# Performance work log

Hardware: AMD Instinct MI355X
Metric: run time of the kernel (lower is better)

The kernel has to match this reference:

```python
import jax, jax.numpy as jnp
import numpy as np

B, S, E, H = 2, 2048, 1024, 16
D = E // H  # head_dim = 64
SCALE = 1.0 / np.sqrt(D)


def setup_inputs() -> dict:
    key = jax.random.key(0)
    ks = jax.random.split(key, 5)
    std = 0.02
    return {
        "x": jax.random.normal(ks[0], (B, S, E), dtype=jnp.float32),
        "wq": jax.random.normal(ks[1], (E, E), dtype=jnp.float32) * std,
        "wk": jax.random.normal(ks[2], (E, E), dtype=jnp.float32) * std,
        "wv": jax.random.normal(ks[3], (E, E), dtype=jnp.float32) * std,
        "wo": jax.random.normal(ks[4], (E, E), dtype=jnp.float32) * std,
    }


def reference(x, wq, wk, wv, wo):
    # Linear projections (torch Linear: y = x @ W.T); weights stored as [out, in]
    q = jnp.einsum('bse,fe->bsf', x, wq)
    k = jnp.einsum('bse,fe->bsf', x, wk)
    v = jnp.einsum('bse,fe->bsf', x, wv)
    # split heads -> [B, H, S, D]
    q = q.reshape(B, S, H, D).transpose(0, 2, 1, 3)
    k = k.reshape(B, S, H, D).transpose(0, 2, 1, 3)
    v = v.reshape(B, S, H, D).transpose(0, 2, 1, 3)
    # scaled dot-product scores [B, H, S, S]
    scores = jnp.einsum('bhqd,bhkd->bhqk', q, k) * SCALE
    # causal mask: -inf above diagonal
    causal = jnp.triu(jnp.full((S, S), -jnp.inf, dtype=scores.dtype), k=1)
    scores = scores + causal[None, None, :, :]
    attn = jax.nn.softmax(scores, axis=-1)
    # dropout p=0 -> identity
    out = jnp.einsum('bhqk,bhkd->bhqd', attn, v)
    out = out.transpose(0, 2, 1, 3).reshape(B, S, E)
    return jnp.einsum('bse,fe->bsf', out, wo)
```

## Files before the change

kernel.cpp:

```cpp
#include <hip/hip_runtime.h>
#include <hip/hip_bf16.h>

#define B_ 2
#define S_ 2048
#define E_ 1024
#define H_ 16
#define D_ 64
#define QKV_N 3072
#define C2_ 0.18033688011112042f

typedef __attribute__((ext_vector_type(8))) unsigned short ushort8_t;
typedef __attribute__((ext_vector_type(8))) short short8_t;
typedef __attribute__((ext_vector_type(4))) float f32x4;

__device__ __forceinline__ unsigned short f2b(float f) {
    union { float f; unsigned u; } x; x.f = f;
    unsigned r = x.u + 0x7FFFu + ((x.u >> 16) & 1u);
    return (unsigned short)(r >> 16);
}
__device__ __forceinline__ ushort2 pkbf(float a, float b) {
    union { __hip_bfloat162 h; ushort2 u; } c;
    c.h = __float22bfloat162_rn(make_float2(a, b));
    return c.u;
}
__device__ __forceinline__ void glds16(const unsigned short* g, unsigned short* l) {
    __builtin_amdgcn_global_load_lds((const __attribute__((address_space(1))) void*)g,
                                     (__attribute__((address_space(3))) void*)l, 16, 0, 0);
}

__global__ __launch_bounds__(256) void cast_all(const float* __restrict__ x,
                                                const float* __restrict__ wq,
                                                const float* __restrict__ wk,
                                                const float* __restrict__ wv,
                                                const float* __restrict__ wo,
                                                unsigned short* __restrict__ xb,
                                                unsigned short* __restrict__ wb) {
    int idx = blockIdx.x * 256 + threadIdx.x;
    const float* src; unsigned short* dst; float s = 1.f; int j;
    if (idx < 1048576) {
        src = x; dst = xb; j = idx;
    } else {
        j = idx - 1048576;
        int y = j >> 18;
        src = (y == 0) ? wq : (y == 1) ? wk : (y == 2) ? wv : wo;
        dst = wb + (size_t)y * 1048576;
        j &= 262143;
        if (y == 0) s = C2_;
    }
    float4 v = ((const float4*)src)[j];
    ushort2 lo = pkbf(v.x * s, v.y * s), hi = pkbf(v.z * s, v.w * s);
    ((ushort4*)dst)[j] = make_ushort4(lo.x, lo.y, hi.x, hi.y);
}

template <int TM, bool OUT_BF16, bool VT>
__device__ __forceinline__ void gemm_bt_body(const unsigned short* __restrict__ A,
                                             const unsigned short* __restrict__ Bt,
                                             void* __restrict__ Cout,
                                             int m0, int n0, int N, int K) {
    __shared__ unsigned short As[2 * TM * 32];
    __shared__ unsigned short Bs[2 * 128 * 32];
    const int tid = threadIdx.x;
    const int wave = tid >> 6;
    const int lane = tid & 63;
    const int wm = (wave >> 1) * (TM / 2);
    const int wn = (wave & 1) * 64;
    const int quad = lane >> 4;
    const int l15 = lane & 15;
    constexpr int MI = TM / 32;

    f32x4 acc[MI][4] = {};

    const int srow = lane >> 2;
    const int scb  = (lane & 3) * 8;
    const unsigned short* gB0 = Bt + (size_t)(n0 + wave * 32 + srow) * K + scb;
    const unsigned short* gB1 = gB0 + (size_t)16 * K;
    unsigned short* lB0 = Bs + wave * 1024;
    unsigned short* lB1 = lB0 + 512;
    const unsigned short* gA0;
    const unsigned short* gA1 = nullptr;
    unsigned short* lA0;
    unsigned short* lA1 = nullptr;
    if (TM == 128) {
        gA0 = A + (size_t)(m0 + wave * 32 + srow) * K + scb;
        gA1 = gA0 + (size_t)16 * K;
        lA0 = As + wave * 1024; lA1 = lA0 + 512;
    } else {
        gA0 = A + (size_t)(m0 + wave * 16 + srow) * K + scb;
        lA0 = As + wave * 512;
    }

    for (int k0 = 0; k0 < K; k0 += 64) {
        __syncthreads();
        glds16(gA0 + k0, lA0);
        glds16(gA0 + k0 + 32, lA0 + TM * 32);
        if (TM == 128) {
            glds16(gA1 + k0, lA1);
            glds16(gA1 + k0 + 32, lA1 + TM * 32);
        }
        glds16(gB0 + k0, lB0);
        glds16(gB0 + k0 + 32, lB0 + 128 * 32);
        glds16(gB1 + k0, lB1);
        glds16(gB1 + k0 + 32, lB1 + 128 * 32);
        __syncthreads();

#pragma unroll
        for (int h = 0; h < 2; ++h) {
            const unsigned short* ah = As + h * TM * 32;
            const unsigned short* bh = Bs + h * 128 * 32;
            short8_t af[MI], bfv[4];
#pragma unroll
            for (int mi = 0; mi < MI; ++mi)
                af[mi] = *(const short8_t*)(&ah[(wm + mi * 16 + l15) * 32 + quad * 8]);
#pragma unroll
            for (int ni = 0; ni < 4; ++ni)
                bfv[ni] = *(const short8_t*)(&bh[(wn + ni * 16 + l15) * 32 + quad * 8]);
#pragma unroll
            for (int mi = 0; mi < MI; ++mi)
#pragma unroll
                for (int ni = 0; ni < 4; ++ni)
                    acc[mi][ni] = __builtin_amdgcn_mfma_f32_16x16x32_bf16(
                        af[mi], bfv[ni], acc[mi][ni], 0, 0, 0);
        }
    }

    if (VT && n0 >= 2048) {
#pragma unroll
        for (int mi = 0; mi < MI; ++mi)
#pragma unroll
            for (int ni = 0; ni < 4; ++ni) {
                int col = n0 + wn + ni * 16 + l15;
                int r0  = m0 + wm + mi * 16 + quad * 4;
                int bb  = r0 >> 11, s = r0 & 2047;
                size_t drow = (size_t)bb * 2048 + 2 * (col - 2048) + (s >> 10);
                unsigned short* dp = (unsigned short*)Cout + drow * QKV_N + 2048 + (s & 1023);
                *(ushort4*)dp = make_ushort4(f2b(acc[mi][ni][0]), f2b(acc[mi][ni][1]),
                                             f2b(acc[mi][ni][2]), f2b(acc[mi][ni][3]));
            }
        return;
    }

#pragma unroll
    for (int mi = 0; mi < MI; ++mi)
#pragma unroll
        for (int ni = 0; ni < 4; ++ni)
#pragma unroll
            for (int r = 0; r < 4; ++r) {
                int row = m0 + wm + mi * 16 + quad * 4 + r;
                int col = n0 + wn + ni * 16 + l15;
                float val = acc[mi][ni][r];
                if (OUT_BF16)
                    ((unsigned short*)Cout)[(size_t)row * N + col] = f2b(val);
                else
                    ((float*)Cout)[(size_t)row * N + col] = val;
            }
}

__global__ __launch_bounds__(256, 3) void gemm_qkv(const unsigned short* __restrict__ xb,
                                                   const unsigned short* __restrict__ wqkv,
                                                   unsigned short* __restrict__ qkv) {
    int id = blockIdx.x + 24 * blockIdx.y;
    int sw = (id & 7) * 96 + (id >> 3);
    int n0 = (sw % 24) * 128;
    int m0 = (sw / 24) * 128;
    gemm_bt_body<128, true, true>(xb, wqkv, qkv, m0, n0, QKV_N, E_);
}

__global__ __launch_bounds__(256, 2) void gemm_out(const unsigned short* __restrict__ a,
                                                   const unsigned short* __restrict__ wob,
                                                   float* __restrict__ c) {
    gemm_bt_body<64, false, false>(a, wob, c, blockIdx.y * 64, blockIdx.x * 128, E_, E_);
}

__global__ __launch_bounds__(512, 4) void attn_kernel(const unsigned short* __restrict__ QKV,
                                                      unsigned short* __restrict__ O) {
    __shared__ unsigned short Ks[2][64 * 64];
    __shared__ unsigned short Vs[2][64 * 64];
    __shared__ unsigned short Ps[8][16 * 64];

    const int b = blockIdx.z, h = blockIdx.y;
    const int cx = blockIdx.x;
    const int c0 = (cx & 1) ? (15 - (cx >> 1)) : (cx >> 1);
    const int c = (b == 0) ? c0 : (15 - c0);
    const int tid = threadIdx.x;
    const int w = tid >> 6, lane = tid & 63;
    const int quad = lane >> 4, l15 = lane & 15;
    const int lx = l15 & 7;
    const int chunk = (w < 4) ? (31 - c) : c;
    const int Q0 = chunk * 64 + (w & 3) * 16;

    const size_t qo = (size_t)(b * S_ + Q0 + l15) * QKV_N + h * D_;
    short8_t bq0 = *(const short8_t*)(QKV + qo + quad * 8);
    short8_t bq1 = *(const short8_t*)(QKV + qo + 32 + quad * 8);

    f32x4 Oacc[4] = {};
    float lsum = 0.f;
    const int qg = Q0 + l15;

    const int fo0 = ((quad) ^ lx) * 8;
    const int fo1 = ((4 + quad) ^ lx) * 8;
    const int krow = l15 * 64;
    int pwo[4];
#pragma unroll
    for (int tm = 0; tm < 4; ++tm)
        pwo[tm] = ((tm * 2 + (quad >> 1)) ^ lx) * 8 + (quad & 1) * 4;

    const int srow = tid >> 3;
    const int scb  = tid & 7;
    const int swz  = (scb ^ (srow & 7)) * 8;
    const unsigned short* Kbase = QKV + (size_t)(b * S_) * QKV_N + 1024 + h * D_;
    const unsigned short* Vb2 = QKV + (size_t)(b * S_ + 2 * (h * D_ + srow)) * QKV_N + 2048;

    const int ntiles = 32 - c;
    const int nT = (ntiles + 1) >> 1;
    for (int t = 0; t < nT; ++t) {
        const int kt0 = t * 128;
        ushort8_t ka = *(const ushort8_t*)(Kbase + (size_t)(kt0 + srow) * QKV_N + scb * 8);
        ushort8_t kb = *(const ushort8_t*)(Kbase + (size_t)(kt0 + 64 + srow) * QKV_N + scb * 8);
        ushort8_t va = *(const ushort8_t*)(Vb2 + (size_t)(kt0 >> 10) * QKV_N
                                               + (kt0 & 1023) + scb * 8);
        ushort8_t vb = *(const ushort8_t*)(Vb2 + (size_t)((kt0 + 64) >> 10) * QKV_N
                                               + ((kt0 + 64) & 1023) + scb * 8);
        __syncthreads();
        *(ushort8_t*)(&Ks[0][srow * 64 + swz]) = ka;
        *(ushort8_t*)(&Ks[1][srow * 64 + swz]) = kb;
        *(ushort8_t*)(&Vs[0][srow * 64 + swz]) = va;
        *(ushort8_t*)(&Vs[1][srow * 64 + swz]) = vb;
        __syncthreads();

#pragma unroll
        for (int s = 0; s < 2; ++s) {
            const int kt = kt0 + s * 64;
            if (kt > Q0 + 15) continue;
            const bool h2 = (kt + 32 <= Q0 + 15);

            if (kt + 63 <= Q0) {
#pragma unroll
                for (int tm = 0; tm < 4; ++tm) {
                    short8_t ak0 = *(const short8_t*)(&Ks[s][tm * 1024 + krow + fo0]);
                    short8_t ak1 = *(const short8_t*)(&Ks[s][tm * 1024 + krow + fo1]);
                    f32x4 st = {0.f, 0.f, 0.f, 0.f};
                    st = __builtin_amdgcn_mfma_f32_16x16x32_bf16(ak0, bq0, st, 0, 0, 0);
                    st = __builtin_amdgcn_mfma_f32_16x16x32_bf16(ak1, bq1, st, 0, 0, 0);
                    float p0 = __builtin_amdgcn_exp2f(st[0]);
                    float p1 = __builtin_amdgcn_exp2f(st[1]);
                    float p2 = __builtin_amdgcn_exp2f(st[2]);
                    float p3 = __builtin_amdgcn_exp2f(st[3]);
                    lsum += (p0 + p1) + (p2 + p3);
                    ushort2 a = pkbf(p0, p1), c2 = pkbf(p2, p3);
                    *(ushort4*)(&Ps[w][krow + pwo[tm]]) = make_ushort4(a.x, a.y, c2.x, c2.y);
                }
            } else {
                const int need = h2 ? 4 : 2;
                for (int tm = 0; tm < need; ++tm) {
                    if (kt + tm * 16 <= Q0 + 15) {
                        short8_t ak0 = *(const short8_t*)(&Ks[s][tm * 1024 + krow + fo0]);
                        short8_t ak1 = *(const short8_t*)(&Ks[s][tm * 1024 + krow + fo1]);
                        f32x4 st = {0.f, 0.f, 0.f, 0.f};
                        st = __builtin_amdgcn_mfma_f32_16x16x32_bf16(ak0, bq0, st, 0, 0, 0);
                        st = __builtin_amdgcn_mfma_f32_16x16x32_bf16(ak1, bq1, st, 0, 0, 0);
                        const int kvb = kt + tm * 16 + quad * 4;
                        float p0 = (kvb     > qg) ? 0.f : __builtin_amdgcn_exp2f(st[0]);
                        float p1 = (kvb + 1 > qg) ? 0.f : __builtin_amdgcn_exp2f(st[1]);
                        float p2 = (kvb + 2 > qg) ? 0.f : __builtin_amdgcn_exp2f(st[2]);
                        float p3 = (kvb + 3 > qg) ? 0.f : __builtin_amdgcn_exp2f(st[3]);
                        lsum += (p0 + p1) + (p2 + p3);
                        ushort2 a = pkbf(p0, p1), c2 = pkbf(p2, p3);
                        *(ushort4*)(&Ps[w][krow + pwo[tm]]) = make_ushort4(a.x, a.y, c2.x, c2.y);
                    } else {
                        *(ushort4*)(&Ps[w][krow + pwo[tm]]) = make_ushort4(0, 0, 0, 0);
                    }
                }
            }

#pragma unroll
            for (int kh = 0; kh < 2; ++kh) {
                if (kh == 1 && !h2) break;
                const int fo = kh ? fo1 : fo0;
                short8_t bv[4];
#pragma unroll
                for (int tn = 0; tn < 4; ++tn)
                    bv[tn] = *(const short8_t*)(&Vs[s][tn * 1024 + krow + fo]);
                short8_t ap = *(const short8_t*)(&Ps[w][krow + fo]);
#pragma unroll
                for (int tn = 0; tn < 4; ++tn)
                    Oacc[tn] = __builtin_amdgcn_mfma_f32_16x16x32_bf16(
                        ap, bv[tn], Oacc[tn], 0, 0, 0);
            }
        }
    }

    float l = lsum;
    l += __shfl_xor(l, 16);
    l += __shfl_xor(l, 32);
    float inv = 1.f / l;
    float lir[4];
#pragma unroll
    for (int r = 0; r < 4; ++r)
        lir[r] = __shfl(inv, quad * 4 + r);
#pragma unroll
    for (int tn = 0; tn < 4; ++tn)
#pragma unroll
        for (int r = 0; r < 4; ++r) {
            int row = Q0 + quad * 4 + r;
            O[(size_t)(b * S_ + row) * E_ + h * D_ + tn * 16 + l15] =
                f2b(Oacc[tn][r] * lir[r]);
        }
}

extern "C" void kernel_launch(void* const* d_in, const int* in_sizes, int n_in,
                              void* d_out, int out_size, void* d_ws, size_t ws_size,
                              hipStream_t stream) {
    const float* x  = (const float*)d_in[0];
    const float* wq = (const float*)d_in[1];
    const float* wk = (const float*)d_in[2];
    const float* wv = (const float*)d_in[3];
    const float* wo = (const float*)d_in[4];
    float* out = (float*)d_out;

    unsigned short* ws   = (unsigned short*)d_ws;
    unsigned short* xb   = ws;
    unsigned short* wqkv = ws + 4194304;
    unsigned short* wob  = ws + 7340032;
    unsigned short* qkvb = ws + 8388608;
    unsigned short* ab   = ws + 20971520;

    cast_all<<<8192, 256, 0, stream>>>(x, wq, wk, wv, wo, xb, wqkv);
    gemm_qkv<<<dim3(24, 32), 256, 0, stream>>>(xb, wqkv, qkvb);
    attn_kernel<<<dim3(16, 16, 2), 512, 0, stream>>>(qkvb, ab);
    gemm_out<<<dim3(8, 64), 256, 0, stream>>>(ab, wob, out);
}
```

Baseline: 169.4 us.

## Double-buffer K/V tiles via direct global-to-LDS loads and compute row sums with MFMA

Replaces the register-staged two-tile load with a 64-row double-buffered pipeline that issues direct global-to-LDS copies (glds16) for the next tile while the current one is computed, removing one barrier per step. The softmax denominator is now computed by an extra MFMA of P against a ones vector instead of scalar adds plus shuffles. MFMA sections are wrapped in setprio hints. This adds one extra MFMA per kv half, sums the bf16-rounded P rather than the fp32 values, and relies on the glds16 helper and the LDS layout matching the wave offset scheme.

```diff
diff --git a/kernel.cpp b/kernel.cpp
--- a/kernel.cpp
+++ b/kernel.cpp
@@ -193,8 +193,11 @@
     short8_t bq1 = *(const short8_t*)(QKV + qo + 32 + quad * 8);
 
     f32x4 Oacc[4] = {};
-    float lsum = 0.f;
+    f32x4 Lacc = {};
     const int qg = Q0 + l15;
+    short8_t ones;
+#pragma unroll
+    for (int i = 0; i < 8; ++i) ones[i] = (short)0x3F80;
 
     const int fo0 = ((quad) ^ lx) * 8;
     const int fo1 = ((4 + quad) ^ lx) * 8;
@@ -206,97 +209,93 @@
 
     const int srow = tid >> 3;
     const int scb  = tid & 7;
-    const int swz  = (scb ^ (srow & 7)) * 8;
-    const unsigned short* Kbase = QKV + (size_t)(b * S_) * QKV_N + 1024 + h * D_;
-    const unsigned short* Vb2 = QKV + (size_t)(b * S_ + 2 * (h * D_ + srow)) * QKV_N + 2048;
+    const int scw  = (scb ^ (srow & 7)) * 8;
+    const int wofs = w * 512;
+    const unsigned short* KsrcB = QKV + (size_t)(b * S_ + srow) * QKV_N + 1024 + h * D_ + scw;
+    const unsigned short* VsrcB = QKV + (size_t)(b * S_ + 2 * (h * D_ + srow)) * QKV_N + 2048 + scw;
+
+    auto issue = [&](int pn, int ktn) {
+        glds16(KsrcB + (size_t)ktn * QKV_N, &Ks[pn][wofs]);
+        glds16(VsrcB + (size_t)(ktn >> 10) * QKV_N + (ktn & 1023), &Vs[pn][wofs]);
+    };
 
     const int ntiles = 32 - c;
-    const int nT = (ntiles + 1) >> 1;
-    for (int t = 0; t < nT; ++t) {
-        const int kt0 = t * 128;
-        ushort8_t ka = *(const ushort8_t*)(Kbase + (size_t)(kt0 + srow) * QKV_N + scb * 8);
-        ushort8_t kb = *(const ushort8_t*)(Kbase + (size_t)(kt0 + 64 + srow) * QKV_N + scb * 8);
-        ushort8_t va = *(const ushort8_t*)(Vb2 + (size_t)(kt0 >> 10) * QKV_N
-                                               + (kt0 & 1023) + scb * 8);
-        ushort8_t vb = *(const ushort8_t*)(Vb2 + (size_t)((kt0 + 64) >> 10) * QKV_N
-                                               + ((kt0 + 64) & 1023) + scb * 8);
+    issue(0, 0);
+
+    for (int t = 0; t < ntiles; ++t) {
+        const int p = t & 1;
+        const int kt = t * 64;
         __syncthreads();
-        *(ushort8_t*)(&Ks[0][srow * 64 + swz]) = ka;
-        *(ushort8_t*)(&Ks[1][srow * 64 + swz]) = kb;
-        *(ushort8_t*)(&Vs[0][srow * 64 + swz]) = va;
-        *(ushort8_t*)(&Vs[1][srow * 64 + swz]) = vb;
-        __syncthreads();
-
-#pragma unroll
-        for (int s = 0; s < 2; ++s) {
-            const int kt = kt0 + s * 64;
-            if (kt > Q0 + 15) continue;
-            const bool h2 = (kt + 32 <= Q0 + 15);
-
-            if (kt + 63 <= Q0) {
-#pragma unroll
-                for (int tm = 0; tm < 4; ++tm) {
-                    short8_t ak0 = *(const short8_t*)(&Ks[s][tm * 1024 + krow + fo0]);
-                    short8_t ak1 = *(const short8_t*)(&Ks[s][tm * 1024 + krow + fo1]);
+        if (t + 1 < ntiles) issue(p ^ 1, kt + 64);
+        __builtin_amdgcn_sched_barrier(0);
+
+        if (kt > Q0 + 15) continue;
+        const bool h2 = (kt + 32 <= Q0 + 15);
+
+        if (kt + 63 <= Q0) {
+#pragma unroll
+            for (int tm = 0; tm < 4; ++tm) {
+                short8_t ak0 = *(const short8_t*)(&Ks[p][tm * 1024 + krow + fo0]);
+                short8_t ak1 = *(const short8_t*)(&Ks[p][tm * 1024 + krow + fo1]);
+                f32x4 st = {0.f, 0.f, 0.f, 0.f};
+                __builtin_amdgcn_s_setprio(1);
+                st = __builtin_amdgcn_mfma_f32_16x16x32_bf16(ak0, bq0, st, 0, 0, 0);
+                st = __builtin_amdgcn_mfma_f32_16x16x32_bf16(ak1, bq1, st, 0, 0, 0);
+                __builtin_amdgcn_s_setprio(0);
+                float p0 = __builtin_amdgcn_exp2f(st[0]);
+                float p1 = __builtin_amdgcn_exp2f(st[1]);
+                float p2 = __builtin_amdgcn_exp2f(st[2]);
+                float p3 = __builtin_amdgcn_exp2f(st[3]);
+                ushort2 a = pkbf(p0, p1), c2 = pkbf(p2, p3);
+                *(ushort4*)(&Ps[w][krow + pwo[tm]]) = make_ushort4(a.x, a.y, c2.x, c2.y);
+            }
+        } else {
+            const int need = h2 ? 4 : 2;
+            for (int tm = 0; tm < need; ++tm) {
+                if (kt + tm * 16 <= Q0 + 15) {
+                    short8_t ak0 = *(const short8_t*)(&Ks[p][tm * 1024 + krow + fo0]);
+                    short8_t ak1 = *(const short8_t*)(&Ks[p][tm * 1024 + krow + fo1]);
                     f32x4 st = {0.f, 0.f, 0.f, 0.f};
+                    __builtin_amdgcn_s_setprio(1);
                     st = __builtin_amdgcn_mfma_f32_16x16x32_bf16(ak0, bq0, st, 0, 0, 0);
                     st = __builtin_amdgcn_mfma_f32_16x16x32_bf16(ak1, bq1, st, 0, 0, 0);
-                    float p0 = __builtin_amdgcn_exp2f(st[0]);
-                    float p1 = __builtin_amdgcn_exp2f(st[1]);
-                    float p2 = __builtin_amdgcn_exp2f(st[2]);
-                    float p3 = __builtin_amdgcn_exp2f(st[3]);
-                    lsum += (p0 + p1) + (p2 + p3);
+                    __builtin_amdgcn_s_setprio(0);
+                    const int kvb = kt + tm * 16 + quad * 4;
+                    float p0 = (kvb     > qg) ? 0.f : __builtin_amdgcn_exp2f(st[0]);
+                    float p1 = (kvb + 1 > qg) ? 0.f : __builtin_amdgcn_exp2f(st[1]);
+                    float p2 = (kvb + 2 > qg) ? 0.f : __builtin_amdgcn_exp2f(st[2]);
+                    float p3 = (kvb + 3 > qg) ? 0.f : __builtin_amdgcn_exp2f(st[3]);
                     ushort2 a = pkbf(p0, p1), c2 = pkbf(p2, p3);
                     *(ushort4*)(&Ps[w][krow + pwo[tm]]) = make_ushort4(a.x, a.y, c2.x, c2.y);
-                }
-            } else {
-                const int need = h2 ? 4 : 2;
-                for (int tm = 0; tm < need; ++tm) {
-                    if (kt + tm * 16 <= Q0 + 15) {
-                        short8_t ak0 = *(const short8_t*)(&Ks[s][tm * 1024 + krow + fo0]);
-                        short8_t ak1 = *(const short8_t*)(&Ks[s][tm * 1024 + krow + fo1]);
-                        f32x4 st = {0.f, 0.f, 0.f, 0.f};
-                        st = __builtin_amdgcn_mfma_f32_16x16x32_bf16(ak0, bq0, st, 0, 0, 0);
-                        st = __builtin_amdgcn_mfma_f32_16x16x32_bf16(ak1, bq1, st, 0, 0, 0);
-                        const int kvb = kt + tm * 16 + quad * 4;
-                        float p0 = (kvb     > qg) ? 0.f : __builtin_amdgcn_exp2f(st[0]);
-                        float p1 = (kvb + 1 > qg) ? 0.f : __builtin_amdgcn_exp2f(st[1]);
-                        float p2 = (kvb + 2 > qg) ? 0.f : __builtin_amdgcn_exp2f(st[2]);
-                        float p3 = (kvb + 3 > qg) ? 0.f : __builtin_amdgcn_exp2f(st[3]);
-                        lsum += (p0 + p1) + (p2 + p3);
-                        ushort2 a = pkbf(p0, p1), c2 = pkbf(p2, p3);
-                        *(ushort4*)(&Ps[w][krow + pwo[tm]]) = make_ushort4(a.x, a.y, c2.x, c2.y);
-                    } else {
-                        *(ushort4*)(&Ps[w][krow + pwo[tm]]) = make_ushort4(0, 0, 0, 0);
-                    }
+                } else {
+                    *(ushort4*)(&Ps[w][krow + pwo[tm]]) = make_ushort4(0, 0, 0, 0);
                 }
             }
-
-#pragma unroll
-            for (int kh = 0; kh < 2; ++kh) {
-                if (kh == 1 && !h2) break;
-                const int fo = kh ? fo1 : fo0;
-                short8_t bv[4];
-#pragma unroll
-                for (int tn = 0; tn < 4; ++tn)
-                    bv[tn] = *(const short8_t*)(&Vs[s][tn * 1024 + krow + fo]);
-                short8_t ap = *(const short8_t*)(&Ps[w][krow + fo]);
-#pragma unroll
-                for (int tn = 0; tn < 4; ++tn)
-                    Oacc[tn] = __builtin_amdgcn_mfma_f32_16x16x32_bf16(
-                        ap, bv[tn], Oacc[tn], 0, 0, 0);
-            }
-        }
-    }
-
-    float l = lsum;
-    l += __shfl_xor(l, 16);
-    l += __shfl_xor(l, 32);
-    float inv = 1.f / l;
+        }
+
+#pragma unroll
+        for (int kh = 0; kh < 2; ++kh) {
+            if (kh == 1 && !h2) break;
+            const int fo = kh ? fo1 : fo0;
+            short8_t bv[4];
+#pragma unroll
+            for (int tn = 0; tn < 4; ++tn)
+                bv[tn] = *(const short8_t*)(&Vs[p][tn * 1024 + krow + fo]);
+            short8_t ap = *(const short8_t*)(&Ps[w][krow + fo]);
+            __builtin_amdgcn_s_setprio(1);
+#pragma unroll
+            for (int tn = 0; tn < 4; ++tn)
+                Oacc[tn] = __builtin_amdgcn_mfma_f32_16x16x32_bf16(
+                    ap, bv[tn], Oacc[tn], 0, 0, 0);
+            Lacc = __builtin_amdgcn_mfma_f32_16x16x32_bf16(ap, ones, Lacc, 0, 0, 0);
+            __builtin_amdgcn_s_setprio(0);
+        }
+    }
+
     float lir[4];
 #pragma unroll
     for (int r = 0; r < 4; ++r)
-        lir[r] = __shfl(inv, quad * 4 + r);
+        lir[r] = 1.f / Lacc[r];
 #pragma unroll
     for (int tn = 0; tn < 4; ++tn)
 #pragma unroll
```

New measurement: 171.2 us. About the same (+1.0%).
